# Performance work log

Hardware: AMD Instinct MI355X
Metric: run time of the kernel (lower is better)

The kernel has to match this reference:

```python
import jax, jax.numpy as jnp
import numpy as np

# dims
BB, T, D_IN = 16, 2048, 64
D = 512          # hidden_dim (d_model)
DI = 2 * D       # d_inner (expand=2)
N = 16           # d_state
DC = 4           # d_conv
R = D // 16      # dt_rank = 32
L = 3            # n_layer
D_OUT = 128


def setup_inputs() -> dict:
    key = jax.random.key(0)
    ks = jax.random.split(key, 10)
    g = lambda k, shape, s: (jax.random.normal(k, shape, jnp.float32) * s)
    A_log = jnp.tile(jnp.log(jnp.arange(1, N + 1, dtype=jnp.float32))[None, None, :], (L, DI, 1))
    return {
        "x": g(ks[0], (BB, T, D_IN), 1.0),
        "Wi": g(ks[1], (D, D_IN), 0.05), "bi": jnp.zeros((D,), jnp.float32),
        "Win": g(ks[2], (L, 2 * DI, D), 0.02),
        "convw": g(ks[3], (L, DI, DC), 0.2), "convb": jnp.zeros((L, DI), jnp.float32),
        "Wx": g(ks[4], (L, R + 2 * N, DI), 0.02),
        "Wdt": g(ks[5], (L, DI, R), 0.05), "bdt": jnp.full((L, DI), -1.0, jnp.float32),
        "A_log": A_log, "Dp": jnp.ones((L, DI), jnp.float32),
        "Wout": g(ks[6], (L, D, DI), 0.02),
        "Wo": g(ks[7], (D_OUT, D), 0.05), "bo": jnp.zeros((D_OUT,), jnp.float32),
    }


def _selective_scan(u, delta, A, Bm, Cm, Dv):
    # u, delta: [B,T,DI]; A: [DI,N]; Bm, Cm: [B,T,N]; Dv: [DI]
    def step(h, inp):
        d_t, u_t, B_t, C_t = inp  # [B,DI],[B,DI],[B,N],[B,N]
        dA = jnp.exp(d_t[:, :, None] * A)                      # [B,DI,N]
        h = dA * h + (d_t * u_t)[:, :, None] * B_t[:, None, :]  # [B,DI,N]
        y = jnp.einsum('bdn,bn->bd', h, C_t)
        return h, y

    h0 = jnp.zeros((u.shape[0], u.shape[2], A.shape[1]), u.dtype)
    xs = (delta.transpose(1, 0, 2), u.transpose(1, 0, 2),
          Bm.transpose(1, 0, 2), Cm.transpose(1, 0, 2))
    _, ys = jax.lax.scan(step, h0, xs)
    return ys.transpose(1, 0, 2) + u * Dv


def _mamba_layer(x, Win, cw, cb, Wx, Wdt, bdt, A_log, Dv, Wout):
    xz = x @ Win.T                      # [B,T,2*DI]
    xin, z = jnp.split(xz, 2, axis=-1)
    # causal depthwise conv1d
    xc = jax.lax.conv_general_dilated(
        xin.transpose(0, 2, 1), cw[:, None, :], (1,), [(DC - 1, 0)],
        feature_group_count=DI, dimension_numbers=('NCH', 'OIH', 'NCH'))
    u = jax.nn.silu((xc + cb[None, :, None]).transpose(0, 2, 1))  # [B,T,DI]
    dbc = u @ Wx.T                      # [B,T,R+2N]
    dt, Bm, Cm = dbc[..., :R], dbc[..., R:R + N], dbc[..., R + N:]
    delta = jax.nn.softplus(dt @ Wdt.T + bdt)
    A = -jnp.exp(A_log)
    y = _selective_scan(u, delta, A, Bm, Cm, Dv)
    return (y * jax.nn.silu(z)) @ Wout.T


def reference(x, Wi, bi, Win, convw, convb, Wx, Wdt, bdt, A_log, Dp, Wout, Wo, bo):
    h = x @ Wi.T + bi
    for l in range(L):
        h = _mamba_layer(h, Win[l], convw[l], convb[l], Wx[l], Wdt[l], bdt[l],
                         A_log[l], Dp[l], Wout[l])
    return jnp.tanh(h @ Wo.T + bo)  # [B,T,output_dim]
```

## Files before the change

kernel.cpp:

```cpp
#include <hip/hip_runtime.h>
#include <hip/hip_bf16.h>

#define BB_ 16
#define T_ 2048
#define DIN_ 64
#define D_ 512
#define DI_ 1024
#define N_ 16
#define DC_ 4
#define R_ 32
#define L_ 3
#define DOUT_ 128
#define CL_ 64
#define NCH_ (T_ / CL_)

typedef __attribute__((ext_vector_type(8))) _Float16 f16x8;
typedef __attribute__((ext_vector_type(4))) float f32x4;

__device__ __forceinline__ float silu_f(float x) { return x / (1.f + __expf(-x)); }

__device__ __forceinline__ float softplus_f(float t) {
    return fmaxf(t, 0.f) + __logf(1.f + __expf(-fabsf(t)));
}

__device__ __forceinline__ unsigned short f2h(float f) {
    union { _Float16 h; unsigned short u; } c;
    c.h = (_Float16)f;
    return c.u;
}

__device__ __forceinline__ void gload_lds16(const unsigned short* g,
                                            unsigned short* l) {
    __builtin_amdgcn_global_load_lds(
        (const __attribute__((address_space(1))) void*)g,
        (__attribute__((address_space(3))) void*)l, 16, 0, 0);
}

__device__ __forceinline__ float decode_scale(unsigned int bits) {
    if (bits == 0u) return 1.f;
    const int E = (int)(bits >> 23) & 0xFF;
    return __uint_as_float((unsigned)(265 - E) << 23);
}

__device__ __forceinline__ uint4 pack8(float4 lo, float4 hi, float s) {
    union { uint4 u; unsigned short h[8]; } r;
    r.h[0] = f2h(lo.x * s); r.h[1] = f2h(lo.y * s);
    r.h[2] = f2h(lo.z * s); r.h[3] = f2h(lo.w * s);
    r.h[4] = f2h(hi.x * s); r.h[5] = f2h(hi.y * s);
    r.h[6] = f2h(hi.z * s); r.h[7] = f2h(hi.w * s);
    return r.u;
}

__device__ __forceinline__ const float* wregion(
    int r, const float* Win, const float* Wout, const float* Wx,
    const float* Wo, size_t* n4)
{
    if (r < 3)       { *n4 = 262144; return Win  + (size_t)r * 1048576; }
    else if (r < 6)  { *n4 = 131072; return Wout + (size_t)(r - 3) * 524288; }
    else if (r == 6) { *n4 = 16384;  return Wo; }
    else             { *n4 = 16384;  return Wx  + (size_t)(r - 7) * 65536; }
}

__global__ __launch_bounds__(256) void amax_all(
    const float* __restrict__ Win, const float* __restrict__ Wout,
    const float* __restrict__ Wx, const float* __restrict__ Wo,
    unsigned int* __restrict__ scales)
{
    size_t n4;
    const float* p = wregion(blockIdx.z, Win, Wout, Wx, Wo, &n4);
    float m = 0.f;
    for (size_t i = (size_t)blockIdx.x * 256 + threadIdx.x; i < n4;
         i += (size_t)gridDim.x * 256) {
        const float4 v = ((const float4*)p)[i];
        m = fmaxf(m, fmaxf(fmaxf(fabsf(v.x), fabsf(v.y)),
                           fmaxf(fabsf(v.z), fabsf(v.w))));
    }
#pragma unroll
    for (int off = 32; off; off >>= 1) m = fmaxf(m, __shfl_down(m, off));
    __shared__ float sm[4];
    if ((threadIdx.x & 63) == 0) sm[threadIdx.x >> 6] = m;
    __syncthreads();
    if (threadIdx.x == 0) {
        const float b = fmaxf(fmaxf(sm[0], sm[1]), fmaxf(sm[2], sm[3]));
        atomicMax(scales + blockIdx.z, __float_as_uint(b));
    }
}

__global__ __launch_bounds__(256) void cast_all(
    const float* __restrict__ Win, const float* __restrict__ Wout,
    const float* __restrict__ Wx, const float* __restrict__ Wo,
    unsigned short* __restrict__ WinH, unsigned short* __restrict__ WoutH,
    unsigned short* __restrict__ WxH, unsigned short* __restrict__ WoH,
    const unsigned int* __restrict__ scales)
{
    const int r = blockIdx.z;
    size_t n4;
    const float* p = wregion(r, Win, Wout, Wx, Wo, &n4);
    unsigned short* o;
    if (r < 3)       o = WinH  + (size_t)r * 1048576;
    else if (r < 6)  o = WoutH + (size_t)(r - 3) * 524288;
    else if (r == 6) o = WoH;
    else             o = WxH   + (size_t)(r - 7) * 65536;
    const float s = decode_scale(scales[r]);
    for (size_t i = (size_t)blockIdx.x * 256 + threadIdx.x; i < n4;
         i += (size_t)gridDim.x * 256) {
        const float4 v = ((const float4*)p)[i];
        ((ushort4*)o)[i] = make_ushort4(f2h(v.x * s), f2h(v.y * s),
                                        f2h(v.z * s), f2h(v.w * s));
    }
}

template<int ACT>
__global__ __launch_bounds__(256) void gemm_f32a_t128(
    const float* __restrict__ A, int lda,
    const unsigned short* __restrict__ B, int ldb,
    const float* __restrict__ bias,
    float* __restrict__ C, int ldc, int K,
    const unsigned int* __restrict__ sa, const unsigned int* __restrict__ sb,
    unsigned int* __restrict__ oamax)
{
    __shared__ __align__(16) unsigned short As[128 * 32];
    __shared__ __align__(16) unsigned short Bs[2][128 * 32];
    const int tid  = threadIdx.x;
    const int lane = tid & 63;
    const int w    = tid >> 6;
    const int wr   = (w >> 1) << 6;
    const int wc   = (w & 1) << 6;
    const int l15  = lane & 15, l4 = lane >> 4;
    const int row0 = blockIdx.y << 7, col0 = blockIdx.x << 7;
    const int tq   = tid >> 2;
    const int tr   = (tid & 3) << 3;

    const float sA  = decode_scale(*sa);
    const float inv = (1.f / sA) * (1.f / decode_scale(*sb));

    const float* Ar0 = A + (size_t)(row0 + tq) * lda + tr;
    const float* Ar1 = A + (size_t)(row0 + 64 + tq) * lda + tr;
    const unsigned short* Br0 = B + (size_t)(col0 + tq) * ldb + tr;
    const unsigned short* Br1 = B + (size_t)(col0 + 64 + tq) * ldb + tr;

    f32x4 acc[4][4];
#pragma unroll
    for (int m = 0; m < 4; ++m)
#pragma unroll
        for (int n = 0; n < 4; ++n) acc[m][n] = (f32x4){0.f, 0.f, 0.f, 0.f};

    float4 a0lo = *(const float4*)(Ar0), a0hi = *(const float4*)(Ar0 + 4);
    float4 a1lo = *(const float4*)(Ar1), a1hi = *(const float4*)(Ar1 + 4);
    gload_lds16(Br0, &Bs[0][tq * 32 + tr]);
    gload_lds16(Br1, &Bs[0][(64 + tq) * 32 + tr]);

    int cur = 0;
    for (int k0 = 0; k0 < K; k0 += 32) {
        __syncthreads();
        *(uint4*)&As[tq * 32 + tr]        = pack8(a0lo, a0hi, sA);
        *(uint4*)&As[(64 + tq) * 32 + tr] = pack8(a1lo, a1hi, sA);
        __syncthreads();

        if (k0 + 32 < K) {
            gload_lds16(Br0 + k0 + 32, &Bs[cur ^ 1][tq * 32 + tr]);
            gload_lds16(Br1 + k0 + 32, &Bs[cur ^ 1][(64 + tq) * 32 + tr]);
            a0lo = *(const float4*)(Ar0 + k0 + 32);
            a0hi = *(const float4*)(Ar0 + k0 + 36);
            a1lo = *(const float4*)(Ar1 + k0 + 32);
            a1hi = *(const float4*)(Ar1 + k0 + 36);
        }

        f16x8 af[4], bfr[4];
#pragma unroll
        for (int m = 0; m < 4; ++m)
            af[m] = *(const f16x8*)&As[(wr + m * 16 + l15) * 32 + l4 * 8];
#pragma unroll
        for (int n = 0; n < 4; ++n)
            bfr[n] = *(const f16x8*)&Bs[cur][(wc + n * 16 + l15) * 32 + l4 * 8];
#pragma unroll
        for (int m = 0; m < 4; ++m)
#pragma unroll
            for (int n = 0; n < 4; ++n)
                acc[m][n] = __builtin_amdgcn_mfma_f32_16x16x32_f16(
                    af[m], bfr[n], acc[m][n], 0, 0, 0);
        cur ^= 1;
    }

    float am = 0.f;
#pragma unroll
    for (int n = 0; n < 4; ++n) {
        const int col = col0 + wc + n * 16 + l15;
        float bc = 0.f;
        if (ACT == 3) bc = bias[col];
#pragma unroll
        for (int m = 0; m < 4; ++m) {
            const int rowb = row0 + wr + m * 16 + (l4 << 2);
#pragma unroll
            for (int r = 0; r < 4; ++r) {
                float v = acc[m][n][r] * inv;
                if (ACT == 3) v = tanhf(v + bc);
                C[(size_t)(rowb + r) * ldc + col] = v;
                am = fmaxf(am, fabsf(v));
            }
        }
    }
    if (oamax) {
#pragma unroll
        for (int off = 32; off; off >>= 1) am = fmaxf(am, __shfl_down(am, off));
        if (lane == 0) atomicMax(oamax, __float_as_uint(am));
    }
}

__global__ __launch_bounds__(256) void gemm_f16u_t64n(
    const float* __restrict__ A, int lda,
    const unsigned short* __restrict__ B, int ldb,
    float* __restrict__ C, int ldc, int K,
    const unsigned int* __restrict__ sa, const unsigned int* __restrict__ sb)
{
    __shared__ __align__(16) unsigned short As[128 * 32];
    __shared__ __align__(16) unsigned short Bs[64 * 32];
    const int tid  = threadIdx.x;
    const int lane = tid & 63;
    const int w    = tid >> 6;
    const int l15  = lane & 15, l4 = lane >> 4;
    const int row0 = blockIdx.y << 7;
    const int tq   = tid >> 2;
    const int tr   = (tid & 3) << 3;

    const float sA  = decode_scale(*sa);
    const float inv = (1.f / sA) * (1.f / decode_scale(*sb));

    const float* Ar0 = A + (size_t)(row0 + tq) * lda + tr;
    const float* Ar1 = A + (size_t)(row0 + 64 + tq) * lda + tr;
    const unsigned short* Br = B + (size_t)tq * ldb + tr;

    f32x4 acc[2][4];
#pragma unroll
    for (int m = 0; m < 2; ++m)
#pragma unroll
        for (int n = 0; n < 4; ++n) acc[m][n] = (f32x4){0.f, 0.f, 0.f, 0.f};

    float4 a0lo = *(const float4*)(Ar0), a0hi = *(const float4*)(Ar0 + 4);
    float4 a1lo = *(const float4*)(Ar1), a1hi = *(const float4*)(Ar1 + 4);
    uint4  bv   = *(const uint4*)(Br);

    for (int k0 = 0; k0 < K; k0 += 32) {
        __syncthreads();
        *(uint4*)&As[tq * 32 + tr]        = pack8(a0lo, a0hi, sA);
        *(uint4*)&As[(64 + tq) * 32 + tr] = pack8(a1lo, a1hi, sA);
        *(uint4*)&Bs[tq * 32 + tr]        = bv;
        __syncthreads();

        if (k0 + 32 < K) {
            a0lo = *(const float4*)(Ar0 + k0 + 32);
            a0hi = *(const float4*)(Ar0 + k0 + 36);
            a1lo = *(const float4*)(Ar1 + k0 + 32);
            a1hi = *(const float4*)(Ar1 + k0 + 36);
            bv   = *(const uint4*)(Br  + k0 + 32);
        }

        f16x8 af[2], bfr[4];
#pragma unroll
        for (int m = 0; m < 2; ++m)
            af[m] = *(const f16x8*)&As[(w * 32 + m * 16 + l15) * 32 + l4 * 8];
#pragma unroll
        for (int n = 0; n < 4; ++n)
            bfr[n] = *(const f16x8*)&Bs[(n * 16 + l15) * 32 + l4 * 8];
#pragma unroll
        for (int m = 0; m < 2; ++m)
#pragma unroll
            for (int n = 0; n < 4; ++n)
                acc[m][n] = __builtin_amdgcn_mfma_f32_16x16x32_f16(
                    af[m], bfr[n], acc[m][n], 0, 0, 0);
    }

#pragma unroll
    for (int n = 0; n < 4; ++n) {
        const int col = n * 16 + l15;
#pragma unroll
        for (int m = 0; m < 2; ++m) {
            const int rowb = row0 + w * 32 + m * 16 + (l4 << 2);
#pragma unroll
            for (int r = 0; r < 4; ++r)
                C[(size_t)(rowb + r) * ldc + col] = acc[m][n][r] * inv;
        }
    }
}

__global__ __launch_bounds__(256) void gemm_in(
    const float* __restrict__ A, int lda,
    const float* __restrict__ B, int ldb,
    const float* __restrict__ bias,
    float* __restrict__ C, int ldc, int K,
    unsigned int* __restrict__ oamax)
{
    __shared__ __align__(16) float As[8][128];
    __shared__ __align__(16) float Bs[8][128];
    const int tid  = threadIdx.x;
    const int row0 = blockIdx.y << 7;
    const int col0 = blockIdx.x << 7;
    const int tx = tid & 15, ty = tid >> 4;

    float acc[8][8];
#pragma unroll
    for (int i = 0; i < 8; ++i)
#pragma unroll
        for (int j = 0; j < 8; ++j) acc[i][j] = 0.f;

    const int arow = tid >> 1;
    const int acol = (tid & 1) << 2;
    const float* Ap = A + (size_t)(row0 + arow) * lda + acol;
    const float* Bp = B + (size_t)(col0 + arow) * ldb + acol;

    for (int k0 = 0; k0 < K; k0 += 8) {
        const float4 av = *(const float4*)(Ap + k0);
        const float4 bv = *(const float4*)(Bp + k0);
        __syncthreads();
        As[acol + 0][arow] = av.x; As[acol + 1][arow] = av.y;
        As[acol + 2][arow] = av.z; As[acol + 3][arow] = av.w;
        Bs[acol + 0][arow] = bv.x; Bs[acol + 1][arow] = bv.y;
        Bs[acol + 2][arow] = bv.z; Bs[acol + 3][arow] = bv.w;
        __syncthreads();
#pragma unroll
        for (int k = 0; k < 8; ++k) {
            float a[8], b[8];
            *(float4*)&a[0] = *(const float4*)&As[k][ty << 3];
            *(float4*)&a[4] = *(const float4*)&As[k][(ty << 3) + 4];
            *(float4*)&b[0] = *(const float4*)&Bs[k][tx << 3];
            *(float4*)&b[4] = *(const float4*)&Bs[k][(tx << 3) + 4];
#pragma unroll
            for (int i = 0; i < 8; ++i)
#pragma unroll
                for (int j = 0; j < 8; ++j)
                    acc[i][j] = fmaf(a[i], b[j], acc[i][j]);
        }
    }

    float bv8[8];
#pragma unroll
    for (int j = 0; j < 8; ++j) bv8[j] = bias[col0 + (tx << 3) + j];

    float am = 0.f;
#pragma unroll
    for (int i = 0; i < 8; ++i) {
        float v[8];
#pragma unroll
        for (int j = 0; j < 8; ++j) {
            v[j] = acc[i][j] + bv8[j];
            am = fmaxf(am, fabsf(v[j]));
        }
        float* Cp = C + (size_t)(row0 + (ty << 3) + i) * ldc + col0 + (tx << 3);
        *(float4*)(Cp)     = make_float4(v[0], v[1], v[2], v[3]);
        *(float4*)(Cp + 4) = make_float4(v[4], v[5], v[6], v[7]);
    }
#pragma unroll
    for (int off = 32; off; off >>= 1) am = fmaxf(am, __shfl_down(am, off));
    if ((tid & 63) == 0) atomicMax(oamax, __float_as_uint(am));
}

__global__ __launch_bounds__(256) void conv_silu_kernel(
    const float* __restrict__ xz, const float* __restrict__ cw,
    const float* __restrict__ cb, float* __restrict__ u,
    size_t total4, unsigned int* __restrict__ uamax)
{
    float am = 0.f;
    for (size_t i = (size_t)blockIdx.x * 256 + threadIdx.x; i < total4;
         i += (size_t)gridDim.x * 256) {
        const size_t e = i * 4;
        const int c = (int)(e & (DI_ - 1));
        const size_t m = e >> 10;
        const int t = (int)(m & (T_ - 1));
        const float* xr = xz + m * 2048 + c;
        const float4 zero = make_float4(0.f, 0.f, 0.f, 0.f);
        const float4 x0 = (t >= 3) ? *(const float4*)(xr - 3 * 2048) : zero;
        const float4 x1 = (t >= 2) ? *(const float4*)(xr - 2 * 2048) : zero;
        const float4 x2 = (t >= 1) ? *(const float4*)(xr - 1 * 2048) : zero;
        const float4 x3 = *(const float4*)(xr);
        const float4 cbv = *(const float4*)(cb + c);
        const float4 w0 = *(const float4*)(cw + (size_t)c * 4);
        const float4 w1 = *(const float4*)(cw + (size_t)(c + 1) * 4);
        const float4 w2 = *(const float4*)(cw + (size_t)(c + 2) * 4);
        const float4 w3 = *(const float4*)(cw + (size_t)(c + 3) * 4);
        float4 r;
        r.x = silu_f(fmaf(x3.x, w0.w, fmaf(x2.x, w0.z, fmaf(x1.x, w0.y, fmaf(x0.x, w0.x, cbv.x)))));
        r.y = silu_f(fmaf(x3.y, w1.w, fmaf(x2.y, w1.z, fmaf(x1.y, w1.y, fmaf(x0.y, w1.x, cbv.y)))));
        r.z = silu_f(fmaf(x3.z, w2.w, fmaf(x2.z, w2.z, fmaf(x1.z, w2.y, fmaf(x0.z, w2.x, cbv.z)))));
        r.w = silu_f(fmaf(x3.w, w3.w, fmaf(x2.w, w3.z, fmaf(x1.w, w3.y, fmaf(x0.w, w3.x, cbv.w)))));
        *(float4*)(u + e) = r;
        am = fmaxf(am, fmaxf(fmaxf(fabsf(r.x), fabsf(r.y)),
                             fmaxf(fabsf(r.z), fabsf(r.w))));
    }
#pragma unroll
    for (int off = 32; off; off >>= 1) am = fmaxf(am, __shfl_down(am, off));
    __shared__ float sm[4];
    if ((threadIdx.x & 63) == 0) sm[threadIdx.x >> 6] = am;
    __syncthreads();
    if (threadIdx.x == 0) {
        const float b = fmaxf(fmaxf(sm[0], sm[1]), fmaxf(sm[2], sm[3]));
        atomicMax(uamax, __float_as_uint(b));
    }
}


__device__ __forceinline__ bool geo_check(const float* a2) {
    bool ok = true;
#pragma unroll
    for (int n = 1; n < N_; ++n)
        ok = ok && (fabsf(a2[n] - a2[0] * (n + 1)) <=
                    1e-5f * fmaxf(1.f, fabsf(a2[n])));
    return ok;
}

__global__ __launch_bounds__(256) void scan_pass1(
    const float* __restrict__ u, const float* __restrict__ dbc,
    const float* __restrict__ A_log_l, const float* __restrict__ Wdt_l,
    const float* __restrict__ bdt_l,
    float* __restrict__ SDL, float* __restrict__ S)
{
    __shared__ __align__(16) float sAll[CL_][64];
    const int tid = threadIdx.x;
    const int b = blockIdx.x, ch = blockIdx.z;
    const int d = (blockIdx.y << 8) + tid;

    float a2[N_], hs[N_];
#pragma unroll
    for (int n = 0; n < N_; ++n) {
        a2[n] = -__expf(A_log_l[d * N_ + n]) * 1.44269504f;
        hs[n] = 0.f;
    }
    const bool geo = geo_check(a2);
    float wdt[32];
#pragma unroll
    for (int k = 0; k < 32; k += 4)
        *(float4*)&wdt[k] = *(const float4*)(Wdt_l + (size_t)d * 32 + k);
    const float bdt_d = bdt_l[d];

    const size_t base64 = ((size_t)b * T_ + (size_t)ch * CL_) * 64;
    float* sflat = &sAll[0][0];
    for (int i = tid; i < CL_ * 64; i += 256) sflat[i] = dbc[base64 + i];
    __syncthreads();

    float sdl = 0.f;
    if (geo) {
        for (int tt = 0; tt < CL_; ++tt) {
            float t = bdt_d;
#pragma unroll
            for (int k = 0; k < 32; k += 4) {
                const float4 dv = *(const float4*)&sAll[tt][k];
                t = fmaf(dv.x, wdt[k + 0], t);
                t = fmaf(dv.y, wdt[k + 1], t);
                t = fmaf(dv.z, wdt[k + 2], t);
                t = fmaf(dv.w, wdt[k + 3], t);
            }
            const float dl = softplus_f(t);
            sdl += dl;
            const size_t m = (size_t)b * T_ + ch * CL_ + tt;
            const float du = dl * u[m * DI_ + d];
            const float r = exp2f(dl * a2[0]);
            float dA = r;
#pragma unroll
            for (int n = 0; n < N_; ++n) {
                hs[n] = fmaf(dA, hs[n], du * sAll[tt][32 + n]);
                dA *= r;
            }
        }
    } else {
        for (int tt = 0; tt < CL_; ++tt) {
            float t = bdt_d;
#pragma unroll
            for (int k = 0; k < 32; k += 4) {
                const float4 dv = *(const float4*)&sAll[tt][k];
                t = fmaf(dv.x, wdt[k + 0], t);
                t = fmaf(dv.y, wdt[k + 1], t);
                t = fmaf(dv.z, wdt[k + 2], t);
                t = fmaf(dv.w, wdt[k + 3], t);
            }
            const float dl = softplus_f(t);
            sdl += dl;
            const size_t m = (size_t)b * T_ + ch * CL_ + tt;
            const float du = dl * u[m * DI_ + d];
#pragma unroll
            for (int n = 0; n < N_; ++n) {
                const float dA = exp2f(dl * a2[n]);
                hs[n] = fmaf(dA, hs[n], du * sAll[tt][32 + n]);
            }
        }
    }
    SDL[(size_t)((b * NCH_ + ch) << 10) + d] = sdl;
#pragma unroll
    for (int n = 0; n < N_; ++n) {
        const size_t idx = (size_t)(((b * NCH_ + ch) * N_ + n) << 10) + d;
        S[idx] = hs[n];
    }
}

__global__ __launch_bounds__(256) void scan_carry(
    const float* __restrict__ SDL, float* __restrict__ S,
    const float* __restrict__ A_log_l)
{
    const size_t gid = (size_t)blockIdx.x * 256 + threadIdx.x;
    const int d = (int)(gid & 1023);
    const int n = (int)((gid >> 10) & 15);
    const int b = (int)(gid >> 14);
    const float a2n = -__expf(A_log_l[d * N_ + n]) * 1.44269504f;
    float hc = 0.f;
    for (int ch = 0; ch < NCH_; ++ch) {
        const float sdl = SDL[(size_t)((b * NCH_ + ch) << 10) + d];
        const float p = exp2f(sdl * a2n);
        const size_t idx = (size_t)(((b * NCH_ + ch) * N_ + n) << 10) + d;
        const float s = S[idx];
        S[idx] = hc;
        hc = fmaf(p, hc, s);
    }
}

__global__ __launch_bounds__(256) void scan_pass3(
    float* __restrict__ xz, const float* __restrict__ u,
    const float* __restrict__ dbc, const float* __restrict__ A_log_l,
    const float* __restrict__ Wdt_l, const float* __restrict__ bdt_l,
    const float* __restrict__ Dp_l, const float* __restrict__ S,
    unsigned int* __restrict__ gmax)
{
    __shared__ __align__(16) float sAll[CL_][64];
    const int tid = threadIdx.x;
    const int b = blockIdx.x, ch = blockIdx.z;
    const int d = (blockIdx.y << 8) + tid;

    float a2[N_], hs[N_];
#pragma unroll
    for (int n = 0; n < N_; ++n) {
        a2[n] = -__expf(A_log_l[d * N_ + n]) * 1.44269504f;
        hs[n] = S[(size_t)(((b * NCH_ + ch) * N_ + n) << 10) + d];
    }
    const bool geo = geo_check(a2);
    float wdt[32];
#pragma unroll
    for (int k = 0; k < 32; k += 4)
        *(float4*)&wdt[k] = *(const float4*)(Wdt_l + (size_t)d * 32 + k);
    const float bdt_d = bdt_l[d];
    const float Dpd = Dp_l[d];

    const size_t base64 = ((size_t)b * T_ + (size_t)ch * CL_) * 64;
    float* sflat = &sAll[0][0];
    for (int i = tid; i < CL_ * 64; i += 256) sflat[i] = dbc[base64 + i];
    __syncthreads();

    float gm = 0.f;
    if (geo) {
        for (int tt = 0; tt < CL_; ++tt) {
            float t = bdt_d;
#pragma unroll
            for (int k = 0; k < 32; k += 4) {
                const float4 dv = *(const float4*)&sAll[tt][k];
                t = fmaf(dv.x, wdt[k + 0], t);
                t = fmaf(dv.y, wdt[k + 1], t);
                t = fmaf(dv.z, wdt[k + 2], t);
                t = fmaf(dv.w, wdt[k + 3], t);
            }
            const float dl = softplus_f(t);
            const size_t m = (size_t)b * T_ + ch * CL_ + tt;
            const float uv = u[m * DI_ + d];
            const float du = dl * uv;
            const float r = exp2f(dl * a2[0]);
            float dA = r;
            float yv = 0.f;
#pragma unroll
            for (int n = 0; n < N_; ++n) {
                hs[n] = fmaf(dA, hs[n], du * sAll[tt][32 + n]);
                yv = fmaf(hs[n], sAll[tt][48 + n], yv);
                dA *= r;
            }
            yv = fmaf(uv, Dpd, yv);
            const float g = yv * silu_f(xz[m * 2048 + DI_ + d]);
            xz[m * 2048 + d] = g;
            gm = fmaxf(gm, fabsf(g));
        }
    } else {
        for (int tt = 0; tt < CL_; ++tt) {
            float t = bdt_d;
#pragma unroll
            for (int k = 0; k < 32; k += 4) {
                const float4 dv = *(const float4*)&sAll[tt][k];
                t = fmaf(dv.x, wdt[k + 0], t);
                t = fmaf(dv.y, wdt[k + 1], t);
                t = fmaf(dv.z, wdt[k + 2], t);
                t = fmaf(dv.w, wdt[k + 3], t);
            }
            const float dl = softplus_f(t);
            const size_t m = (size_t)b * T_ + ch * CL_ + tt;
            const float uv = u[m * DI_ + d];
            const float du = dl * uv;
            float yv = 0.f;
#pragma unroll
            for (int n = 0; n < N_; ++n) {
                const float dA = exp2f(dl * a2[n]);
                hs[n] = fmaf(dA, hs[n], du * sAll[tt][32 + n]);
                yv = fmaf(hs[n], sAll[tt][48 + n], yv);
            }
            yv = fmaf(uv, Dpd, yv);
            const float g = yv * silu_f(xz[m * 2048 + DI_ + d]);
            xz[m * 2048 + d] = g;
            gm = fmaxf(gm, fabsf(g));
        }
    }
#pragma unroll
    for (int off = 32; off; off >>= 1) gm = fmaxf(gm, __shfl_down(gm, off));
    if ((tid & 63) == 0) atomicMax(gmax, __float_as_uint(gm));
}

extern "C" void kernel_launch(void* const* d_in, const int* in_sizes, int n_in,
                              void* d_out, int out_size, void* d_ws, size_t ws_size,
                              hipStream_t stream) {
    const float* x     = (const float*)d_in[0];
    const float* Wi    = (const float*)d_in[1];
    const float* bi    = (const float*)d_in[2];
    const float* Win   = (const float*)d_in[3];
    const float* convw = (const float*)d_in[4];
    const float* convb = (const float*)d_in[5];
    const float* Wx    = (const float*)d_in[6];
    const float* Wdt   = (const float*)d_in[7];
    const float* bdt   = (const float*)d_in[8];
    const float* A_log = (const float*)d_in[9];
    const float* Dp    = (const float*)d_in[10];
    const float* Wout  = (const float*)d_in[11];
    const float* Wo    = (const float*)d_in[12];
    const float* bo    = (const float*)d_in[13];
    float* out = (float*)d_out;

    const size_t rowf = 3648;
    const size_t wextra =
        (3 * 1048576 + 3 * 524288 + 65536 + 3 * 65536) / 2 + 32;
    int CB = BB_;
    while (CB > 1 && ((size_t)CB * T_ * rowf + wextra) * sizeof(float) > ws_size) CB >>= 1;
    const size_t Mc = (size_t)CB * T_;

    const dim3 blk(256);
    const int rowTiles = (int)(Mc / 128);

    float* ws   = (float*)d_ws;
    float* xz   = ws;
    float* u    = xz + Mc * 2048;
    float* dbc  = u  + Mc * 1024;
    float* hPS  = dbc + Mc * 64;
    float* hb   = hPS;
    float* Sdl  = hPS;
    float* Sbuf = hPS + Mc * 16;
    unsigned short* WinH  = (unsigned short*)(hPS + Mc * 512);
    unsigned short* WoutH = WinH + 3 * 1048576;
    unsigned short* WoH   = WoutH + 3 * 524288;
    unsigned short* WxH   = WoH + 65536;
    unsigned int* scales  = (unsigned int*)(WxH + 3 * 65536);

    hipMemsetAsync(scales, 0, 32 * sizeof(unsigned int), stream);

    amax_all<<<dim3(128, 1, 10), blk, 0, stream>>>(Win, Wout, Wx, Wo, scales);
    cast_all<<<dim3(64, 1, 10), blk, 0, stream>>>(
        Win, Wout, Wx, Wo, WinH, WoutH, WxH, WoH, scales);

    for (int c = 0; c < BB_ / CB; ++c) {
        const float* x_c = x + (size_t)c * Mc * DIN_;
        float* out_c     = out + (size_t)c * Mc * DOUT_;

        hipMemsetAsync(scales + 10, 0, 10 * sizeof(unsigned int), stream);

        gemm_in<<<dim3(D_ / 128, rowTiles), blk, 0, stream>>>(
            x_c, DIN_, Wi, DIN_, bi, hb, D_, DIN_, scales + 10);

        for (int l = 0; l < L_; ++l) {
            const float* cw_l   = convw + (size_t)l * DI_ * DC_;
            const float* cb_l   = convb + (size_t)l * DI_;
            const float* Wdt_l  = Wdt  + (size_t)l * DI_ * R_;
            const float* bdt_l  = bdt  + (size_t)l * DI_;
            const float* Alog_l = A_log + (size_t)l * DI_ * N_;
            const float* Dp_l   = Dp   + (size_t)l * DI_;

            gemm_f32a_t128<0><<<dim3(2048 / 128, rowTiles), blk, 0, stream>>>(
                hb, D_, WinH + (size_t)l * 1048576, D_, nullptr,
                xz, 2048, D_, scales + 10 + l, scales + l, nullptr);

            conv_silu_kernel<<<dim3(2048), blk, 0, stream>>>(
                xz, cw_l, cb_l, u, Mc * DI_ / 4, scales + 17 + l);

            gemm_f16u_t64n<<<dim3(1, rowTiles), blk, 0, stream>>>(
                u, DI_, WxH + (size_t)l * 65536, DI_, dbc, 64, DI_,
                scales + 17 + l, scales + 7 + l);

            scan_pass1<<<dim3(CB, DI_ / 256, NCH_), blk, 0, stream>>>(
                u, dbc, Alog_l, Wdt_l, bdt_l, Sdl, Sbuf);
            scan_carry<<<dim3(CB * 64), blk, 0, stream>>>(Sdl, Sbuf, Alog_l);
            scan_pass3<<<dim3(CB, DI_ / 256, NCH_), blk, 0, stream>>>(
                xz, u, dbc, Alog_l, Wdt_l, bdt_l, Dp_l, Sbuf, scales + 14 + l);

            gemm_f32a_t128<0><<<dim3(D_ / 128, rowTiles), blk, 0, stream>>>(
                xz, 2048, WoutH + (size_t)l * 524288, DI_, nullptr,
                hb, D_, DI_, scales + 14 + l, scales + 3 + l, scales + 11 + l);
        }

        gemm_f32a_t128<3><<<dim3(DOUT_ / 128, rowTiles), blk, 0, stream>>>(
            hb, D_, WoH, D_, bo, out_c, DOUT_, D_,
            scales + 13, scales + 6, nullptr);
    }
}
```

Measured before the change: 2.582 ms.

## Store conv output u as scaled fp16 using an analytic amax bound

The conv+SiLU output u is now stored as scaled fp16 instead of fp32. Its scale comes from an upper bound computed in a tiny kernel from the in-projection GEMM's output amax and the conv weights and bias, so conv no longer reduces its own amax. The Wx GEMM reads fp16 directly without packing, and both scan passes dequantize u on load, halving u traffic. The price is one extra small launch, fp16 precision loss on u in the scan's D skip term, and a looser, conservative scale bound.

```diff
diff --git a/kernel.cpp b/kernel.cpp
--- a/kernel.cpp
+++ b/kernel.cpp
@@ -27,6 +27,12 @@
     union { _Float16 h; unsigned short u; } c;
     c.h = (_Float16)f;
     return c.u;
+}
+
+__device__ __forceinline__ float h2f(unsigned short u) {
+    union { unsigned short u; _Float16 h; } c;
+    c.u = u;
+    return (float)c.h;
 }
 
 __device__ __forceinline__ void gload_lds16(const unsigned short* g,
@@ -110,6 +116,28 @@
     }
 }
 
+__global__ __launch_bounds__(256) void ubound_kernel(
+    const float* __restrict__ cw, const float* __restrict__ cb,
+    const unsigned int* __restrict__ xzslot, unsigned int* __restrict__ uslot)
+{
+    const float amx = __uint_as_float(*xzslot);
+    float m = 0.f;
+    for (int c = threadIdx.x; c < DI_; c += 256) {
+        const float4 w = *(const float4*)(cw + (size_t)c * 4);
+        const float sw = fabsf(w.x) + fabsf(w.y) + fabsf(w.z) + fabsf(w.w);
+        m = fmaxf(m, fabsf(cb[c]) + sw * amx);
+    }
+#pragma unroll
+    for (int off = 32; off; off >>= 1) m = fmaxf(m, __shfl_down(m, off));
+    __shared__ float sm[4];
+    if ((threadIdx.x & 63) == 0) sm[threadIdx.x >> 6] = m;
+    __syncthreads();
+    if (threadIdx.x == 0) {
+        const float b = fmaxf(fmaxf(sm[0], sm[1]), fmaxf(sm[2], sm[3]));
+        atomicMax(uslot, __float_as_uint(b));
+    }
+}
+
 template<int ACT>
 __global__ __launch_bounds__(256) void gemm_f32a_t128(
     const float* __restrict__ A, int lda,
@@ -207,8 +235,8 @@
     }
 }
 
-__global__ __launch_bounds__(256) void gemm_f16u_t64n(
-    const float* __restrict__ A, int lda,
+__global__ __launch_bounds__(256) void gemm_f16_t64n(
+    const unsigned short* __restrict__ A, int lda,
     const unsigned short* __restrict__ B, int ldb,
     float* __restrict__ C, int ldc, int K,
     const unsigned int* __restrict__ sa, const unsigned int* __restrict__ sb)
@@ -223,12 +251,11 @@
     const int tq   = tid >> 2;
     const int tr   = (tid & 3) << 3;
 
-    const float sA  = decode_scale(*sa);
-    const float inv = (1.f / sA) * (1.f / decode_scale(*sb));
-
-    const float* Ar0 = A + (size_t)(row0 + tq) * lda + tr;
-    const float* Ar1 = A + (size_t)(row0 + 64 + tq) * lda + tr;
-    const unsigned short* Br = B + (size_t)tq * ldb + tr;
+    const float inv = (1.f / decode_scale(*sa)) * (1.f / decode_scale(*sb));
+
+    const unsigned short* Ar0 = A + (size_t)(row0 + tq) * lda + tr;
+    const unsigned short* Ar1 = A + (size_t)(row0 + 64 + tq) * lda + tr;
+    const unsigned short* Br  = B + (size_t)tq * ldb + tr;
 
     f32x4 acc[2][4];
 #pragma unroll
@@ -236,23 +263,21 @@
 #pragma unroll
         for (int n = 0; n < 4; ++n) acc[m][n] = (f32x4){0.f, 0.f, 0.f, 0.f};
 
-    float4 a0lo = *(const float4*)(Ar0), a0hi = *(const float4*)(Ar0 + 4);
-    float4 a1lo = *(const float4*)(Ar1), a1hi = *(const float4*)(Ar1 + 4);
-    uint4  bv   = *(const uint4*)(Br);
+    uint4 av0 = *(const uint4*)(Ar0);
+    uint4 av1 = *(const uint4*)(Ar1);
+    uint4 bv  = *(const uint4*)(Br);
 
     for (int k0 = 0; k0 < K; k0 += 32) {
         __syncthreads();
-        *(uint4*)&As[tq * 32 + tr]        = pack8(a0lo, a0hi, sA);
-        *(uint4*)&As[(64 + tq) * 32 + tr] = pack8(a1lo, a1hi, sA);
+        *(uint4*)&As[tq * 32 + tr]        = av0;
+        *(uint4*)&As[(64 + tq) * 32 + tr] = av1;
         *(uint4*)&Bs[tq * 32 + tr]        = bv;
         __syncthreads();
 
         if (k0 + 32 < K) {
-            a0lo = *(const float4*)(Ar0 + k0 + 32);
-            a0hi = *(const float4*)(Ar0 + k0 + 36);
-            a1lo = *(const float4*)(Ar1 + k0 + 32);
-            a1hi = *(const float4*)(Ar1 + k0 + 36);
-            bv   = *(const uint4*)(Br  + k0 + 32);
+            av0 = *(const uint4*)(Ar0 + k0 + 32);
+            av1 = *(const uint4*)(Ar1 + k0 + 32);
+            bv  = *(const uint4*)(Br  + k0 + 32);
         }
 
         f16x8 af[2], bfr[4];
@@ -356,10 +381,10 @@
 
 __global__ __launch_bounds__(256) void conv_silu_kernel(
     const float* __restrict__ xz, const float* __restrict__ cw,
-    const float* __restrict__ cb, float* __restrict__ u,
-    size_t total4, unsigned int* __restrict__ uamax)
-{
-    float am = 0.f;
+    const float* __restrict__ cb, unsigned short* __restrict__ u,
+    size_t total4, const unsigned int* __restrict__ uslot)
+{
+    const float s = decode_scale(*uslot);
     for (size_t i = (size_t)blockIdx.x * 256 + threadIdx.x; i < total4;
          i += (size_t)gridDim.x * 256) {
         const size_t e = i * 4;
@@ -382,18 +407,8 @@
         r.y = silu_f(fmaf(x3.y, w1.w, fmaf(x2.y, w1.z, fmaf(x1.y, w1.y, fmaf(x0.y, w1.x, cbv.y)))));
         r.z = silu_f(fmaf(x3.z, w2.w, fmaf(x2.z, w2.z, fmaf(x1.z, w2.y, fmaf(x0.z, w2.x, cbv.z)))));
         r.w = silu_f(fmaf(x3.w, w3.w, fmaf(x2.w, w3.z, fmaf(x1.w, w3.y, fmaf(x0.w, w3.x, cbv.w)))));
-        *(float4*)(u + e) = r;
-        am = fmaxf(am, fmaxf(fmaxf(fabsf(r.x), fabsf(r.y)),
-                             fmaxf(fabsf(r.z), fabsf(r.w))));
-    }
-#pragma unroll
-    for (int off = 32; off; off >>= 1) am = fmaxf(am, __shfl_down(am, off));
-    __shared__ float sm[4];
-    if ((threadIdx.x & 63) == 0) sm[threadIdx.x >> 6] = am;
-    __syncthreads();
-    if (threadIdx.x == 0) {
-        const float b = fmaxf(fmaxf(sm[0], sm[1]), fmaxf(sm[2], sm[3]));
-        atomicMax(uamax, __float_as_uint(b));
+        *(ushort4*)(u + e) = make_ushort4(f2h(r.x * s), f2h(r.y * s),
+                                          f2h(r.z * s), f2h(r.w * s));
     }
 }
 
@@ -408,9 +423,9 @@
 }
 
 __global__ __launch_bounds__(256) void scan_pass1(
-    const float* __restrict__ u, const float* __restrict__ dbc,
+    const unsigned short* __restrict__ u, const float* __restrict__ dbc,
     const float* __restrict__ A_log_l, const float* __restrict__ Wdt_l,
-    const float* __restrict__ bdt_l,
+    const float* __restrict__ bdt_l, const unsigned int* __restrict__ uslot,
     float* __restrict__ SDL, float* __restrict__ S)
 {
     __shared__ __align__(16) float sAll[CL_][64];
@@ -425,6 +440,7 @@
         hs[n] = 0.f;
     }
     const bool geo = geo_check(a2);
+    const float invU = 1.f / decode_scale(*uslot);
     float wdt[32];
 #pragma unroll
     for (int k = 0; k < 32; k += 4)
@@ -451,7 +467,7 @@
             const float dl = softplus_f(t);
             sdl += dl;
             const size_t m = (size_t)b * T_ + ch * CL_ + tt;
-            const float du = dl * u[m * DI_ + d];
+            const float du = dl * (h2f(u[m * DI_ + d]) * invU);
             const float r = exp2f(dl * a2[0]);
             float dA = r;
 #pragma unroll
@@ -474,7 +490,7 @@
             const float dl = softplus_f(t);
             sdl += dl;
             const size_t m = (size_t)b * T_ + ch * CL_ + tt;
-            const float du = dl * u[m * DI_ + d];
+            const float du = dl * (h2f(u[m * DI_ + d]) * invU);
 #pragma unroll
             for (int n = 0; n < N_; ++n) {
                 const float dA = exp2f(dl * a2[n]);
@@ -511,11 +527,11 @@
 }
 
 __global__ __launch_bounds__(256) void scan_pass3(
-    float* __restrict__ xz, const float* __restrict__ u,
+    float* __restrict__ xz, const unsigned short* __restrict__ u,
     const float* __restrict__ dbc, const float* __restrict__ A_log_l,
     const float* __restrict__ Wdt_l, const float* __restrict__ bdt_l,
-    const float* __restrict__ Dp_l, const float* __restrict__ S,
-    unsigned int* __restrict__ gmax)
+    const float* __restrict__ Dp_l, const unsigned int* __restrict__ uslot,
+    const float* __restrict__ S, unsigned int* __restrict__ gmax)
 {
     __shared__ __align__(16) float sAll[CL_][64];
     const int tid = threadIdx.x;
@@ -529,6 +545,7 @@
         hs[n] = S[(size_t)(((b * NCH_ + ch) * N_ + n) << 10) + d];
     }
     const bool geo = geo_check(a2);
+    const float invU = 1.f / decode_scale(*uslot);
     float wdt[32];
 #pragma unroll
     for (int k = 0; k < 32; k += 4)
@@ -555,7 +572,7 @@
             }
             const float dl = softplus_f(t);
             const size_t m = (size_t)b * T_ + ch * CL_ + tt;
-            const float uv = u[m * DI_ + d];
+            const float uv = h2f(u[m * DI_ + d]) * invU;
             const float du = dl * uv;
             const float r = exp2f(dl * a2[0]);
             float dA = r;
@@ -584,7 +601,7 @@
             }
             const float dl = softplus_f(t);
             const size_t m = (size_t)b * T_ + ch * CL_ + tt;
-            const float uv = u[m * DI_ + d];
+            const float uv = h2f(u[m * DI_ + d]) * invU;
             const float du = dl * uv;
             float yv = 0.f;
 #pragma unroll
@@ -635,8 +652,9 @@
 
     float* ws   = (float*)d_ws;
     float* xz   = ws;
-    float* u    = xz + Mc * 2048;
-    float* dbc  = u  + Mc * 1024;
+    float* uf   = xz + Mc * 2048;
+    unsigned short* ub = (unsigned short*)uf;
+    float* dbc  = uf + Mc * 512;
     float* hPS  = dbc + Mc * 64;
     float* hb   = hPS;
     float* Sdl  = hPS;
@@ -657,7 +675,7 @@
         const float* x_c = x + (size_t)c * Mc * DIN_;
         float* out_c     = out + (size_t)c * Mc * DOUT_;
 
-        hipMemsetAsync(scales + 10, 0, 10 * sizeof(unsigned int), stream);
+        hipMemsetAsync(scales + 10, 0, 16 * sizeof(unsigned int), stream);
 
         gemm_in<<<dim3(D_ / 128, rowTiles), blk, 0, stream>>>(
             x_c, DIN_, Wi, DIN_, bi, hb, D_, DIN_, scales + 10);
@@ -672,20 +690,24 @@
 
             gemm_f32a_t128<0><<<dim3(2048 / 128, rowTiles), blk, 0, stream>>>(
                 hb, D_, WinH + (size_t)l * 1048576, D_, nullptr,
-                xz, 2048, D_, scales + 10 + l, scales + l, nullptr);
+                xz, 2048, D_, scales + 10 + l, scales + l, scales + 17 + l);
+
+            ubound_kernel<<<dim3(1), blk, 0, stream>>>(
+                cw_l, cb_l, scales + 17 + l, scales + 20 + l);
 
             conv_silu_kernel<<<dim3(2048), blk, 0, stream>>>(
-                xz, cw_l, cb_l, u, Mc * DI_ / 4, scales + 17 + l);
-
-            gemm_f16u_t64n<<<dim3(1, rowTiles), blk, 0, stream>>>(
-                u, DI_, WxH + (size_t)l * 65536, DI_, dbc, 64, DI_,
-                scales + 17 + l, scales + 7 + l);
+                xz, cw_l, cb_l, ub, Mc * DI_ / 4, scales + 20 + l);
+
+            gemm_f16_t64n<<<dim3(1, rowTiles), blk, 0, stream>>>(
+                ub, DI_, WxH + (size_t)l * 65536, DI_, dbc, 64, DI_,
+                scales + 20 + l, scales + 7 + l);
 
             scan_pass1<<<dim3(CB, DI_ / 256, NCH_), blk, 0, stream>>>(
-                u, dbc, Alog_l, Wdt_l, bdt_l, Sdl, Sbuf);
+                ub, dbc, Alog_l, Wdt_l, bdt_l, scales + 20 + l, Sdl, Sbuf);
             scan_carry<<<dim3(CB * 64), blk, 0, stream>>>(Sdl, Sbuf, Alog_l);
             scan_pass3<<<dim3(CB, DI_ / 256, NCH_), blk, 0, stream>>>(
-                xz, u, dbc, Alog_l, Wdt_l, bdt_l, Dp_l, Sbuf, scales + 14 + l);
+                xz, ub, dbc, Alog_l, Wdt_l, bdt_l, Dp_l, scales + 20 + l,
+                Sbuf, scales + 14 + l);
 
             gemm_f32a_t128<0><<<dim3(D_ / 128, rowTiles), blk, 0, stream>>>(
                 xz, 2048, WoutH + (size_t)l * 524288, DI_, nullptr,
```

New measurement: 2.870 ms. +11.2%, slower.
